# Kernel tuning notes

Hardware: AMD Instinct MI355X
Metric: run time of the kernel (lower is better)

## Reference

```python
import jax, jax.numpy as jnp
import numpy as np

N = 2048            # new query tokens in this chunk
CHUNK_START = 2048  # tokens already in the KV cache
SLOTS = 8192        # total cache slots
H = 32              # query heads
KVH = 8             # kv heads (GQA)
HD = 128            # head dim
SCALE = float(1.0 / np.sqrt(HD))


def setup_inputs() -> dict:
    key = jax.random.key(0)
    ks = jax.random.split(key, 5)
    q = jax.random.normal(ks[0], (N, H, HD), dtype=jnp.float32)
    k = jax.random.normal(ks[1], (N, KVH, HD), dtype=jnp.float32)
    v = jax.random.normal(ks[2], (N, KVH, HD), dtype=jnp.float32)
    # cache pre-filled with the prior chunk's keys/values (rest is scratch)
    k_cache = jax.random.normal(ks[3], (SLOTS, KVH, HD), dtype=jnp.float32)
    v_cache = jax.random.normal(ks[4], (SLOTS, KVH, HD), dtype=jnp.float32)
    slot_mapping = jnp.arange(N, dtype=jnp.int32) + CHUNK_START
    return {"q": q, "k": k, "v": v, "k_cache": k_cache, "v_cache": v_cache,
            "slot_mapping": slot_mapping, "chunk_start": CHUNK_START}


def reference(q, k, v, k_cache, v_cache, slot_mapping, chunk_start):
    # --- store_kvcache: scatter new k/v rows into the paged cache ---
    kc = k_cache.at[slot_mapping].set(k)
    vc = v_cache.at[slot_mapping].set(v)

    n_q = q.shape[0]
    total_len = chunk_start + n_q  # python int -> static shapes

    # --- GQA: expand kv heads to query heads (repeat_interleave, dim=1) ---
    rep = q.shape[1] // kc.shape[1]
    k_all = jnp.repeat(kc[:total_len], rep, axis=1)  # [T, H, HD]
    v_all = jnp.repeat(vc[:total_len], rep, axis=1)  # [T, H, HD]

    # --- offset causal mask: query i attends to keys <= chunk_start + i ---
    q_pos = jnp.arange(chunk_start, total_len)[:, None]   # [N, 1]
    k_pos = jnp.arange(total_len)[None, :]                # [1, T]
    neg = jnp.finfo(q.dtype).min
    mask = jnp.where(k_pos <= q_pos, jnp.zeros((), q.dtype), neg)  # [N, T]

    # --- scaled dot-product attention ---
    scores = jnp.einsum('qhd,khd->hqk', q, k_all) * SCALE + mask[None]  # [H, N, T]
    attn = jax.nn.softmax(scores, axis=-1)
    out = jnp.einsum('hqk,khd->qhd', attn, v_all)  # [N, H, HD]
    return out
```

## Files before the change

kernel.cpp:

```cpp
#include <hip/hip_runtime.h>

#define H_    32
#define KVH_  8
#define HD_   128
#define CHUNK_ 2048
#define BQ    128
#define BK    64
#define LKS   (HD_ + 8)
#define LVS   (BK + 8)

typedef short bf16x8 __attribute__((ext_vector_type(8)));
typedef float f32x16 __attribute__((ext_vector_type(16)));

__device__ __forceinline__ ushort f2bf(float x) {
  unsigned u = __builtin_bit_cast(unsigned, x);
  u += 0x7FFFu + ((u >> 16) & 1u);
  return (ushort)(u >> 16);
}

__device__ __forceinline__ unsigned cvt_pk_bf16(float a, float b) {
  unsigned r;
  asm("v_cvt_pk_bf16_f32 %0, %1, %2" : "=v"(r) : "v"(a), "v"(b));
  return r;
}

__global__ void prep_kv(const float* __restrict__ k, const float* __restrict__ v,
                        float* __restrict__ kc, float* __restrict__ vc,
                        ushort* __restrict__ Kb, ushort* __restrict__ Vt,
                        const int* __restrict__ slots, int T) {
  __shared__ ushort tile[64 * 128];
  int t0  = blockIdx.x * 64;
  int kvh = blockIdx.y;
  int tid = threadIdx.x;
  int tr = tid >> 5, c4 = tid & 31;
  bool isnew = (t0 >= CHUNK_);
#pragma unroll
  for (int itr = 0; itr < 8; ++itr) {
    int t  = itr * 8 + tr;
    int tg = t0 + t;
    const float* ksrc = isnew ? (k  + (((size_t)(tg - CHUNK_) * KVH_ + kvh) << 7))
                              : (kc + (((size_t)tg * KVH_ + kvh) << 7));
    const float* vsrc = isnew ? (v  + (((size_t)(tg - CHUNK_) * KVH_ + kvh) << 7))
                              : (vc + (((size_t)tg * KVH_ + kvh) << 7));
    float4 kx = *(const float4*)(ksrc + (c4 << 2));
    float4 vx = *(const float4*)(vsrc + (c4 << 2));
    if (isnew) {
      int slot = slots[tg - CHUNK_];
      *(float4*)(kc + (((size_t)slot * KVH_ + kvh) << 7) + (c4 << 2)) = kx;
      *(float4*)(vc + (((size_t)slot * KVH_ + kvh) << 7) + (c4 << 2)) = vx;
    }
    ushort4 ky = make_ushort4(f2bf(kx.x), f2bf(kx.y), f2bf(kx.z), f2bf(kx.w));
    *(ushort4*)&Kb[(((size_t)kvh * T + tg) << 7) + (c4 << 2)] = ky;
    ushort4 vy = make_ushort4(f2bf(vx.x), f2bf(vx.y), f2bf(vx.z), f2bf(vx.w));
    *(ushort4*)&tile[t * 128 + (c4 << 2)] = vy;
  }
  __syncthreads();
  int d = tid >> 1, half = tid & 1;
  unsigned wb[16];
#pragma unroll
  for (int j = 0; j < 16; ++j) {
    unsigned lo = tile[(half * 32 + 2 * j) * 128 + d];
    unsigned hi = tile[(half * 32 + 2 * j + 1) * 128 + d];
    wb[j] = lo | (hi << 16);
  }
  uint4* dst = (uint4*)&Vt[((size_t)(kvh * 128 + d)) * T + t0 + half * 32];
  dst[0] = make_uint4(wb[0],  wb[1],  wb[2],  wb[3]);
  dst[1] = make_uint4(wb[4],  wb[5],  wb[6],  wb[7]);
  dst[2] = make_uint4(wb[8],  wb[9],  wb[10], wb[11]);
  dst[3] = make_uint4(wb[12], wb[13], wb[14], wb[15]);
}

__global__ void conv_q(const float* __restrict__ q, ushort* __restrict__ Qb, int N) {
  const float sc = 0.08838834764831845f * 1.4426950408889634f;
  int idx = blockIdx.x * 256 + threadIdx.x;
  int e = idx << 2;
  int n = e >> 12;
  int h = (e >> 7) & 31;
  int d = e & 127;
  float4 x = ((const float4*)q)[idx];
  ushort4 y = make_ushort4(f2bf(x.x * sc), f2bf(x.y * sc), f2bf(x.z * sc), f2bf(x.w * sc));
  *(ushort4*)&Qb[(((size_t)h * N + n) << 7) + d] = y;
}

__global__ __launch_bounds__(256, 2)
void fa_kernel(const ushort* __restrict__ Qb, const ushort* __restrict__ Kb,
               const ushort* __restrict__ Vt, float* __restrict__ out,
               int N, int T, int nq) {
  __shared__ ushort lK[2][BK * LKS];
  __shared__ ushort lV[2][HD_ * LVS];

  int h = blockIdx.x;
  int j = blockIdx.y;
  int half_q = (nq + 1) >> 1;
  int qt = (j < half_q) ? (2 * j) : (2 * (nq - j) - 1);
  int q0 = qt * BQ;
  int kvh = h >> 2;
  int tid = threadIdx.x;
  int w = tid >> 6, lane = tid & 63;
  int l31 = lane & 31, hi = lane >> 5;

  bf16x8 qf[8];
  const ushort* qb = Qb + (((size_t)h * N + q0 + (w << 5) + l31) << 7);
#pragma unroll
  for (int kt = 0; kt < 8; ++kt)
    qf[kt] = *(const bf16x8*)(qb + (kt << 4) + (hi << 3));

  f32x16 o[4];
#pragma unroll
  for (int dt = 0; dt < 4; ++dt)
#pragma unroll
    for (int r = 0; r < 16; ++r) o[dt][r] = 0.f;
  float m_r = -1e30f, l_r = 0.f;

  int tmax = CHUNK_ + q0 + BQ; if (tmax > T) tmax = T;
  int ntiles = (tmax + BK - 1) >> 6;

  const ushort* kbase = Kb + (((size_t)kvh * T) << 7);
  const ushort* vbase = Vt + ((size_t)kvh << 7) * T;

  bf16x8 kst[4], vst[4];

#pragma unroll
  for (int jj = 0; jj < 4; ++jj) {
    int i = (jj << 8) + tid;
    kst[jj] = *(const bf16x8*)(kbase + ((size_t)(i >> 4) << 7) + ((i & 15) << 3));
    vst[jj] = *(const bf16x8*)(vbase + (size_t)(i >> 3) * T + ((i & 7) << 3));
  }
#pragma unroll
  for (int jj = 0; jj < 4; ++jj) {
    int i = (jj << 8) + tid;
    *(bf16x8*)&lK[0][(i >> 4) * LKS + ((i & 15) << 3)] = kst[jj];
    *(bf16x8*)&lV[0][(i >> 3) * LVS + ((i & 7) << 3)] = vst[jj];
  }
  __syncthreads();

  for (int it = 0; it < ntiles; ++it) {
    int t0 = it << 6;
    int cur = it & 1;
    bool pre = (it + 1) < ntiles;

    if (pre) {
      int t0n = t0 + BK;
      const ushort* kb_t = kbase + ((size_t)t0n << 7);
      const ushort* vb_t = vbase + t0n;
#pragma unroll
      for (int jj = 0; jj < 4; ++jj) {
        int i = (jj << 8) + tid;
        kst[jj] = *(const bf16x8*)(kb_t + ((size_t)(i >> 4) << 7) + ((i & 15) << 3));
      }
#pragma unroll
      for (int jj = 0; jj < 4; ++jj) {
        int i = (jj << 8) + tid;
        vst[jj] = *(const bf16x8*)(vb_t + (size_t)(i >> 3) * T + ((i & 7) << 3));
      }
      __builtin_amdgcn_sched_barrier(0);
    }

    f32x16 s[2];
#pragma unroll
    for (int nt = 0; nt < 2; ++nt)
#pragma unroll
      for (int r = 0; r < 16; ++r) s[nt][r] = 0.f;
    __builtin_amdgcn_s_setprio(1);
#pragma unroll
    for (int nt = 0; nt < 2; ++nt) {
#pragma unroll
      for (int kt = 0; kt < 8; ++kt) {
        bf16x8 kf = *(const bf16x8*)&lK[cur][((nt << 5) + l31) * LKS + (kt << 4) + (hi << 3)];
        s[nt] = __builtin_amdgcn_mfma_f32_32x32x16_bf16(kf, qf[kt], s[nt], 0, 0, 0);
      }
    }
    __builtin_amdgcn_s_setprio(0);

    int qg = q0 + (w << 5) + l31;
    bool need_mask = (t0 + BK - 1) > (CHUNK_ + q0 + (w << 5));
    float mxa = -1e30f, mxb = -1e30f;
    if (need_mask) {
      int lim = CHUNK_ + qg;
#pragma unroll
      for (int nt = 0; nt < 2; ++nt) {
        int tb = t0 + (nt << 5) + (hi << 2);
#pragma unroll
        for (int r = 0; r < 16; ++r) {
          int tg = tb + (r & 3) + ((r >> 2) << 3);
          float sv = s[nt][r];
          if (tg > lim) sv = -3e38f;
          s[nt][r] = sv;
          if (r & 1) mxb = fmaxf(mxb, sv); else mxa = fmaxf(mxa, sv);
        }
      }
    } else {
#pragma unroll
      for (int nt = 0; nt < 2; ++nt)
#pragma unroll
        for (int r = 0; r < 16; ++r) {
          if (r & 1) mxb = fmaxf(mxb, s[nt][r]); else mxa = fmaxf(mxa, s[nt][r]);
        }
    }
    float mx = fmaxf(mxa, mxb);
    mx = fmaxf(mx, __shfl_xor(mx, 32, 64));

    if (__any(mx > m_r + 8.0f)) {
      float mnew  = fmaxf(m_r, mx);
      float alpha = exp2f(m_r - mnew);
      m_r = mnew;
      l_r *= alpha;
#pragma unroll
      for (int dt = 0; dt < 4; ++dt)
#pragma unroll
        for (int r = 0; r < 16; ++r) o[dt][r] *= alpha;
    }

    float s0 = 0.f, s1 = 0.f, s2 = 0.f, s3 = 0.f;
#pragma unroll
    for (int nt = 0; nt < 2; ++nt)
#pragma unroll
      for (int r = 0; r < 16; ++r) {
        float p = exp2f(s[nt][r] - m_r);
        s[nt][r] = p;
        switch (r & 3) {
          case 0: s0 += p; break;
          case 1: s1 += p; break;
          case 2: s2 += p; break;
          default: s3 += p; break;
        }
      }
    float sum = (s0 + s1) + (s2 + s3);
    sum += __shfl_xor(sum, 32, 64);
    l_r += sum;

    bf16x8 pf[4];
#pragma unroll
    for (int c = 0; c < 4; ++c) {
      const int nt = c >> 1, b = (c & 1) << 3;
      unsigned u0 = cvt_pk_bf16(s[nt][b + 0], s[nt][b + 1]);
      unsigned u1 = cvt_pk_bf16(s[nt][b + 2], s[nt][b + 3]);
      unsigned w0 = cvt_pk_bf16(s[nt][b + 4], s[nt][b + 5]);
      unsigned w1 = cvt_pk_bf16(s[nt][b + 6], s[nt][b + 7]);
      unsigned u0s = (unsigned)__shfl_xor((int)u0, 32, 64);
      unsigned u1s = (unsigned)__shfl_xor((int)u1, 32, 64);
      unsigned w0s = (unsigned)__shfl_xor((int)w0, 32, 64);
      unsigned w1s = (unsigned)__shfl_xor((int)w1, 32, 64);
      union { unsigned u[4]; bf16x8 v; } cv;
      cv.u[0] = hi ? w0s : u0;
      cv.u[1] = hi ? w1s : u1;
      cv.u[2] = hi ? w0  : u0s;
      cv.u[3] = hi ? w1  : u1s;
      pf[c] = cv.v;
    }

    __builtin_amdgcn_s_setprio(1);
#pragma unroll
    for (int dt = 0; dt < 4; ++dt) {
#pragma unroll
      for (int kt = 0; kt < 4; ++kt) {
        bf16x8 vf = *(const bf16x8*)&lV[cur][((dt << 5) + l31) * LVS + (kt << 4) + (hi << 3)];
        o[dt] = __builtin_amdgcn_mfma_f32_32x32x16_bf16(vf, pf[kt], o[dt], 0, 0, 0);
      }
    }
    __builtin_amdgcn_s_setprio(0);

    if (pre) {
      int nxt = cur ^ 1;
#pragma unroll
      for (int jj = 0; jj < 4; ++jj) {
        int i = (jj << 8) + tid;
        *(bf16x8*)&lK[nxt][(i >> 4) * LKS + ((i & 15) << 3)] = kst[jj];
        *(bf16x8*)&lV[nxt][(i >> 3) * LVS + ((i & 7) << 3)] = vst[jj];
      }
      __syncthreads();
    }
  }

  {
    int qg = q0 + (w << 5) + l31;
    float inv = 1.0f / l_r;
    float* ob = out + (((size_t)qg * H_ + h) << 7) + (hi << 2);
#pragma unroll
    for (int dt = 0; dt < 4; ++dt)
#pragma unroll
      for (int rq = 0; rq < 4; ++rq) {
        float4 val = make_float4(o[dt][4 * rq + 0] * inv, o[dt][4 * rq + 1] * inv,
                                 o[dt][4 * rq + 2] * inv, o[dt][4 * rq + 3] * inv);
        *(float4*)(ob + (dt << 5) + (rq << 3)) = val;
      }
  }
}

extern "C" void kernel_launch(void* const* d_in, const int* in_sizes, int n_in,
                              void* d_out, int out_size, void* d_ws, size_t ws_size,
                              hipStream_t stream) {
  const float* q  = (const float*)d_in[0];
  const float* k  = (const float*)d_in[1];
  const float* v  = (const float*)d_in[2];
  float* kc       = (float*)d_in[3];
  float* vc       = (float*)d_in[4];
  const int* slots = (const int*)d_in[5];

  int N  = in_sizes[5];
  int T  = CHUNK_ + N;
  int nq = N / BQ;

  ushort* Qb = (ushort*)d_ws;
  ushort* Kb = Qb + (size_t)H_ * N * HD_;
  ushort* Vt = Kb + (size_t)KVH_ * T * HD_;
  float* out = (float*)d_out;

  prep_kv<<<dim3(T / 64, KVH_), 256, 0, stream>>>(k, v, kc, vc, Kb, Vt, slots, T);
  conv_q<<<(N * H_ * HD_) / 1024, 256, 0, stream>>>(q, Qb, N);
  fa_kernel<<<dim3(H_, nq), 256, 0, stream>>>(Qb, Kb, Vt, out, N, T, nq);
}
```

Measured before the change: 305.4 us.

## Fuse Q conversion into attention kernel and software-pipeline QK with softmax-PV

Removes the separate conv_q kernel and instead loads fp32 Q directly in the attention kernel, scaling and packing it to bf16 in registers. This drops one launch and one round trip of Q through global memory. The main loop is restructured into a two-stage software pipeline that computes the next tile's QK^T MFMAs before the current tile's softmax and PV, hoping to overlap matrix work with exp and shuffle work. This keeps two score accumulators live, which raises register pressure, and adds extra barriers. The loop handles tiles in pairs, so an odd tile count could process a tile that was never loaded.

```diff
diff --git a/kernel.cpp b/kernel.cpp
--- a/kernel.cpp
+++ b/kernel.cpp
@@ -70,20 +70,8 @@
   dst[3] = make_uint4(wb[12], wb[13], wb[14], wb[15]);
 }
 
-__global__ void conv_q(const float* __restrict__ q, ushort* __restrict__ Qb, int N) {
-  const float sc = 0.08838834764831845f * 1.4426950408889634f;
-  int idx = blockIdx.x * 256 + threadIdx.x;
-  int e = idx << 2;
-  int n = e >> 12;
-  int h = (e >> 7) & 31;
-  int d = e & 127;
-  float4 x = ((const float4*)q)[idx];
-  ushort4 y = make_ushort4(f2bf(x.x * sc), f2bf(x.y * sc), f2bf(x.z * sc), f2bf(x.w * sc));
-  *(ushort4*)&Qb[(((size_t)h * N + n) << 7) + d] = y;
-}
-
 __global__ __launch_bounds__(256, 2)
-void fa_kernel(const ushort* __restrict__ Qb, const ushort* __restrict__ Kb,
+void fa_kernel(const float* __restrict__ q, const ushort* __restrict__ Kb,
                const ushort* __restrict__ Vt, float* __restrict__ out,
                int N, int T, int nq) {
   __shared__ ushort lK[2][BK * LKS];
@@ -99,11 +87,22 @@
   int w = tid >> 6, lane = tid & 63;
   int l31 = lane & 31, hi = lane >> 5;
 
+  const float sc = 0.08838834764831845f * 1.4426950408889634f;
   bf16x8 qf[8];
-  const ushort* qb = Qb + (((size_t)h * N + q0 + (w << 5) + l31) << 7);
-#pragma unroll
-  for (int kt = 0; kt < 8; ++kt)
-    qf[kt] = *(const bf16x8*)(qb + (kt << 4) + (hi << 3));
+  {
+    const float* qrow = q + (((size_t)(q0 + (w << 5) + l31) * H_ + h) << 7);
+#pragma unroll
+    for (int kt = 0; kt < 8; ++kt) {
+      float4 a = *(const float4*)(qrow + (kt << 4) + (hi << 3));
+      float4 b = *(const float4*)(qrow + (kt << 4) + (hi << 3) + 4);
+      union { unsigned u[4]; bf16x8 v; } cv;
+      cv.u[0] = cvt_pk_bf16(a.x * sc, a.y * sc);
+      cv.u[1] = cvt_pk_bf16(a.z * sc, a.w * sc);
+      cv.u[2] = cvt_pk_bf16(b.x * sc, b.y * sc);
+      cv.u[3] = cvt_pk_bf16(b.z * sc, b.w * sc);
+      qf[kt] = cv.v;
+    }
+  }
 
   f32x16 o[4];
 #pragma unroll
@@ -113,88 +112,77 @@
   float m_r = -1e30f, l_r = 0.f;
 
   int tmax = CHUNK_ + q0 + BQ; if (tmax > T) tmax = T;
-  int ntiles = (tmax + BK - 1) >> 6;
+  int ntl = (tmax + BK - 1) >> 6;
 
   const ushort* kbase = Kb + (((size_t)kvh * T) << 7);
   const ushort* vbase = Vt + ((size_t)kvh << 7) * T;
 
   bf16x8 kst[4], vst[4];
-
-#pragma unroll
-  for (int jj = 0; jj < 4; ++jj) {
-    int i = (jj << 8) + tid;
-    kst[jj] = *(const bf16x8*)(kbase + ((size_t)(i >> 4) << 7) + ((i & 15) << 3));
-    vst[jj] = *(const bf16x8*)(vbase + (size_t)(i >> 3) * T + ((i & 7) << 3));
-  }
-#pragma unroll
-  for (int jj = 0; jj < 4; ++jj) {
-    int i = (jj << 8) + tid;
-    *(bf16x8*)&lK[0][(i >> 4) * LKS + ((i & 15) << 3)] = kst[jj];
-    *(bf16x8*)&lV[0][(i >> 3) * LVS + ((i & 7) << 3)] = vst[jj];
-  }
-  __syncthreads();
-
-  for (int it = 0; it < ntiles; ++it) {
-    int t0 = it << 6;
-    int cur = it & 1;
-    bool pre = (it + 1) < ntiles;
-
-    if (pre) {
-      int t0n = t0 + BK;
-      const ushort* kb_t = kbase + ((size_t)t0n << 7);
-      const ushort* vb_t = vbase + t0n;
-#pragma unroll
-      for (int jj = 0; jj < 4; ++jj) {
-        int i = (jj << 8) + tid;
-        kst[jj] = *(const bf16x8*)(kb_t + ((size_t)(i >> 4) << 7) + ((i & 15) << 3));
-      }
-#pragma unroll
-      for (int jj = 0; jj < 4; ++jj) {
-        int i = (jj << 8) + tid;
-        vst[jj] = *(const bf16x8*)(vb_t + (size_t)(i >> 3) * T + ((i & 7) << 3));
-      }
-      __builtin_amdgcn_sched_barrier(0);
-    }
-
-    f32x16 s[2];
-#pragma unroll
-    for (int nt = 0; nt < 2; ++nt)
-#pragma unroll
-      for (int r = 0; r < 16; ++r) s[nt][r] = 0.f;
+  f32x16 sA[2], sB[2];
+
+  auto ISSUE = [&](int t) {
+    int tt = t << 6;
+    const ushort* kb_t = kbase + ((size_t)tt << 7);
+    const ushort* vb_t = vbase + tt;
+#pragma unroll
+    for (int jj = 0; jj < 4; ++jj) {
+      int i = (jj << 8) + tid;
+      kst[jj] = *(const bf16x8*)(kb_t + ((size_t)(i >> 4) << 7) + ((i & 15) << 3));
+    }
+#pragma unroll
+    for (int jj = 0; jj < 4; ++jj) {
+      int i = (jj << 8) + tid;
+      vst[jj] = *(const bf16x8*)(vb_t + (size_t)(i >> 3) * T + ((i & 7) << 3));
+    }
+    __builtin_amdgcn_sched_barrier(0);
+  };
+  auto WLDS = [&](int b) {
+#pragma unroll
+    for (int jj = 0; jj < 4; ++jj) {
+      int i = (jj << 8) + tid;
+      *(bf16x8*)&lK[b][(i >> 4) * LKS + ((i & 15) << 3)] = kst[jj];
+      *(bf16x8*)&lV[b][(i >> 3) * LVS + ((i & 7) << 3)] = vst[jj];
+    }
+  };
+  auto QKF = [&](const ushort* lKb, f32x16* s) {
+#pragma unroll
+    for (int nt2 = 0; nt2 < 2; ++nt2)
+#pragma unroll
+      for (int r = 0; r < 16; ++r) s[nt2][r] = 0.f;
     __builtin_amdgcn_s_setprio(1);
 #pragma unroll
-    for (int nt = 0; nt < 2; ++nt) {
+    for (int nt2 = 0; nt2 < 2; ++nt2)
 #pragma unroll
       for (int kt = 0; kt < 8; ++kt) {
-        bf16x8 kf = *(const bf16x8*)&lK[cur][((nt << 5) + l31) * LKS + (kt << 4) + (hi << 3)];
-        s[nt] = __builtin_amdgcn_mfma_f32_32x32x16_bf16(kf, qf[kt], s[nt], 0, 0, 0);
-      }
-    }
+        bf16x8 kf = *(const bf16x8*)&lKb[((nt2 << 5) + l31) * LKS + (kt << 4) + (hi << 3)];
+        s[nt2] = __builtin_amdgcn_mfma_f32_32x32x16_bf16(kf, qf[kt], s[nt2], 0, 0, 0);
+      }
     __builtin_amdgcn_s_setprio(0);
-
+  };
+  auto SMPV = [&](f32x16* s, int tt0, const ushort* lVb) {
     int qg = q0 + (w << 5) + l31;
-    bool need_mask = (t0 + BK - 1) > (CHUNK_ + q0 + (w << 5));
+    bool need_mask = (tt0 + BK - 1) > (CHUNK_ + q0 + (w << 5));
     float mxa = -1e30f, mxb = -1e30f;
     if (need_mask) {
       int lim = CHUNK_ + qg;
 #pragma unroll
-      for (int nt = 0; nt < 2; ++nt) {
-        int tb = t0 + (nt << 5) + (hi << 2);
+      for (int nt2 = 0; nt2 < 2; ++nt2) {
+        int tb = tt0 + (nt2 << 5) + (hi << 2);
 #pragma unroll
         for (int r = 0; r < 16; ++r) {
           int tg = tb + (r & 3) + ((r >> 2) << 3);
-          float sv = s[nt][r];
+          float sv = s[nt2][r];
           if (tg > lim) sv = -3e38f;
-          s[nt][r] = sv;
+          s[nt2][r] = sv;
           if (r & 1) mxb = fmaxf(mxb, sv); else mxa = fmaxf(mxa, sv);
         }
       }
     } else {
 #pragma unroll
-      for (int nt = 0; nt < 2; ++nt)
+      for (int nt2 = 0; nt2 < 2; ++nt2)
 #pragma unroll
         for (int r = 0; r < 16; ++r) {
-          if (r & 1) mxb = fmaxf(mxb, s[nt][r]); else mxa = fmaxf(mxa, s[nt][r]);
+          if (r & 1) mxb = fmaxf(mxb, s[nt2][r]); else mxa = fmaxf(mxa, s[nt2][r]);
         }
     }
     float mx = fmaxf(mxa, mxb);
@@ -213,11 +201,11 @@
 
     float s0 = 0.f, s1 = 0.f, s2 = 0.f, s3 = 0.f;
 #pragma unroll
-    for (int nt = 0; nt < 2; ++nt)
+    for (int nt2 = 0; nt2 < 2; ++nt2)
 #pragma unroll
       for (int r = 0; r < 16; ++r) {
-        float p = exp2f(s[nt][r] - m_r);
-        s[nt][r] = p;
+        float p = exp2f(s[nt2][r] - m_r);
+        s[nt2][r] = p;
         switch (r & 3) {
           case 0: s0 += p; break;
           case 1: s1 += p; break;
@@ -232,11 +220,11 @@
     bf16x8 pf[4];
 #pragma unroll
     for (int c = 0; c < 4; ++c) {
-      const int nt = c >> 1, b = (c & 1) << 3;
-      unsigned u0 = cvt_pk_bf16(s[nt][b + 0], s[nt][b + 1]);
-      unsigned u1 = cvt_pk_bf16(s[nt][b + 2], s[nt][b + 3]);
-      unsigned w0 = cvt_pk_bf16(s[nt][b + 4], s[nt][b + 5]);
-      unsigned w1 = cvt_pk_bf16(s[nt][b + 6], s[nt][b + 7]);
+      const int nt2 = c >> 1, b = (c & 1) << 3;
+      unsigned u0 = cvt_pk_bf16(s[nt2][b + 0], s[nt2][b + 1]);
+      unsigned u1 = cvt_pk_bf16(s[nt2][b + 2], s[nt2][b + 3]);
+      unsigned w0 = cvt_pk_bf16(s[nt2][b + 4], s[nt2][b + 5]);
+      unsigned w1 = cvt_pk_bf16(s[nt2][b + 6], s[nt2][b + 7]);
       unsigned u0s = (unsigned)__shfl_xor((int)u0, 32, 64);
       unsigned u1s = (unsigned)__shfl_xor((int)u1, 32, 64);
       unsigned w0s = (unsigned)__shfl_xor((int)w0, 32, 64);
@@ -251,25 +239,35 @@
 
     __builtin_amdgcn_s_setprio(1);
 #pragma unroll
-    for (int dt = 0; dt < 4; ++dt) {
+    for (int dt = 0; dt < 4; ++dt)
 #pragma unroll
       for (int kt = 0; kt < 4; ++kt) {
-        bf16x8 vf = *(const bf16x8*)&lV[cur][((dt << 5) + l31) * LVS + (kt << 4) + (hi << 3)];
+        bf16x8 vf = *(const bf16x8*)&lVb[((dt << 5) + l31) * LVS + (kt << 4) + (hi << 3)];
         o[dt] = __builtin_amdgcn_mfma_f32_32x32x16_bf16(vf, pf[kt], o[dt], 0, 0, 0);
       }
-    }
     __builtin_amdgcn_s_setprio(0);
-
-    if (pre) {
-      int nxt = cur ^ 1;
-#pragma unroll
-      for (int jj = 0; jj < 4; ++jj) {
-        int i = (jj << 8) + tid;
-        *(bf16x8*)&lK[nxt][(i >> 4) * LKS + ((i & 15) << 3)] = kst[jj];
-        *(bf16x8*)&lV[nxt][(i >> 3) * LVS + ((i & 7) << 3)] = vst[jj];
-      }
-      __syncthreads();
-    }
+  };
+
+  ISSUE(0);
+  WLDS(0);
+  __syncthreads();
+  ISSUE(1);
+  QKF(lK[0], sA);
+  WLDS(1);
+  __syncthreads();
+
+  for (int it = 0; it < ntl; it += 2) {
+    bool p2 = (it + 2) < ntl, p3 = (it + 3) < ntl;
+    if (p2) ISSUE(it + 2);
+    QKF(lK[1], sB);
+    SMPV(sA, it << 6, lV[0]);
+    __syncthreads();
+    if (p2) { WLDS(0); __syncthreads(); }
+    if (p3) ISSUE(it + 3);
+    if (p2) QKF(lK[0], sA);
+    SMPV(sB, (it + 1) << 6, lV[1]);
+    __syncthreads();
+    if (p3) { WLDS(1); __syncthreads(); }
   }
 
   {
@@ -301,12 +299,10 @@
   int T  = CHUNK_ + N;
   int nq = N / BQ;
 
-  ushort* Qb = (ushort*)d_ws;
-  ushort* Kb = Qb + (size_t)H_ * N * HD_;
+  ushort* Kb = (ushort*)d_ws;
   ushort* Vt = Kb + (size_t)KVH_ * T * HD_;
   float* out = (float*)d_out;
 
   prep_kv<<<dim3(T / 64, KVH_), 256, 0, stream>>>(k, v, kc, vc, Kb, Vt, slots, T);
-  conv_q<<<(N * H_ * HD_) / 1024, 256, 0, stream>>>(q, Qb, N);
-  fa_kernel<<<dim3(H_, nq), 256, 0, stream>>>(Qb, Kb, Vt, out, N, T, nq);
-}
+  fa_kernel<<<dim3(H_, nq), 256, 0, stream>>>(q, Kb, Vt, out, N, T, nq);
+}
```

After: 308.1 us. No clear change (+0.9%).
